# Optimization experiments

Hardware: AMD Instinct MI355X
Metric: run time of the kernel (lower is better)

The kernel has to match this reference:

```python
import jax, jax.numpy as jnp
import numpy as np

B, C, T, H, K = 512, 64, 512, 128, 16
EPS_BN = 1e-5


def setup_inputs() -> dict:
    key = jax.random.key(0)
    ks = jax.random.split(key, 8)
    s = 0.05
    return {
        "x": jax.random.normal(ks[0], (B, C, T), jnp.float32),
        "conv1_w": jax.random.normal(ks[1], (H, C, 3), jnp.float32) * s,
        "conv1_b": jnp.zeros((H,), jnp.float32),
        "conv2_w": jax.random.normal(ks[2], (H, H, 3), jnp.float32) * s,
        "conv2_b": jnp.zeros((H,), jnp.float32),
        "bnt1_g": jnp.ones((H,), jnp.float32), "bnt1_b": jnp.zeros((H,), jnp.float32),
        "bnt2_g": jnp.ones((H,), jnp.float32), "bnt2_b": jnp.zeros((H,), jnp.float32),
        "W1": jax.random.normal(ks[3], (T, H), jnp.float32) * s, "b1": jnp.zeros((H,), jnp.float32),
        "g1": jnp.ones((H,), jnp.float32), "be1": jnp.zeros((H,), jnp.float32),
        "W2": jax.random.normal(ks[4], (H, H), jnp.float32) * s, "b2": jnp.zeros((H,), jnp.float32),
        "g2": jnp.ones((H,), jnp.float32), "be2": jnp.zeros((H,), jnp.float32),
        "W3": jax.random.normal(ks[5], (H, H), jnp.float32) * s, "b3": jnp.zeros((H,), jnp.float32),
        "g3": jnp.ones((H,), jnp.float32), "be3": jnp.zeros((H,), jnp.float32),
    }


def _bn_nc(z, g, b):
    # BatchNorm1d on (N, C) with batch statistics (training-mode normalization)
    m = z.mean(0)
    v = z.var(0)
    return (z - m) * jax.lax.rsqrt(v + EPS_BN) * g + b


def _bn_ncl(z, g, b):
    # BatchNorm1d on (N, C, L)
    m = z.mean((0, 2), keepdims=True)
    v = z.var((0, 2), keepdims=True)
    return (z - m) * jax.lax.rsqrt(v + EPS_BN) * g[None, :, None] + b[None, :, None]


def _conv1d(z, w, b):
    y = jax.lax.conv_general_dilated(z, w, (1,), "SAME",
                                     dimension_numbers=("NCH", "OIH", "NCH"))
    return y + b[None, :, None]


def _forward(x, conv1_w, conv1_b, conv2_w, conv2_b, bnt1_g, bnt1_b, bnt2_g, bnt2_b,
             W1, b1, g1, be1, W2, b2, g2, be2, W3, b3, g3, be3):
    # temporal branch: computed but unused in the output (faithful to the source)
    ht = jax.nn.relu(_bn_ncl(_conv1d(x, conv1_w, conv1_b), bnt1_g, bnt1_b))
    ht = jax.nn.relu(_bn_ncl(_conv1d(ht, conv2_w, conv2_b), bnt2_g, bnt2_b))

    # dynamic graph: cosine similarity averaged over batch, top-k neighbors per channel
    xn = x / jnp.maximum(jnp.linalg.norm(x, axis=2, keepdims=True), 1e-12)
    sim = jnp.einsum("bct,bdt->cd", xn, xn) / x.shape[0]  # (C, C)
    _, nbr = jax.lax.top_k(sim, K)                        # (C, K)
    src = jnp.repeat(jnp.arange(C), K)                    # (C*K,)
    dst = nbr.reshape(-1)                                 # (C*K,)
    offs = (jnp.arange(B) * C)[:, None]
    N = B * C
    sl = jnp.arange(N)
    # edge_index[0]=source node i, edge_index[1]=its top-k neighbor; plus GCN self-loops
    es = jnp.concatenate([(src[None, :] + offs).reshape(-1), sl])
    ed = jnp.concatenate([(dst[None, :] + offs).reshape(-1), sl])

    deg = jax.ops.segment_sum(jnp.ones(es.shape[0], x.dtype), ed, num_segments=N)
    dinv = jax.lax.rsqrt(deg)  # deg >= 1 due to self-loops
    enorm = dinv[es] * dinv[ed]

    def gcn(h, W, b):
        hw = h @ W
        return jax.ops.segment_sum(hw[es] * enorm[:, None], ed, num_segments=N) + b

    # source does permute(0,2,1).view(B*C, T): a flat reshape of the (B, T, C) tensor
    nodes = jnp.transpose(x, (0, 2, 1)).reshape(N, T)
    h = jax.nn.relu(_bn_nc(gcn(nodes, W1, b1), g1, be1))
    h = jax.nn.relu(_bn_nc(gcn(h, W2, b2), g2, be2))
    h = jax.nn.relu(_bn_nc(gcn(h, W3, b3), g3, be3))
    return h.reshape(B, C * H)


def reference(x, conv1_w, conv1_b, conv2_w, conv2_b, bnt1_g, bnt1_b, bnt2_g, bnt2_b,
              W1, b1, g1, be1, W2, b2, g2, be2, W3, b3, g3, be3):
    return _forward(x, conv1_w, conv1_b, conv2_w, conv2_b, bnt1_g, bnt1_b,
                    bnt2_g, bnt2_b, W1, b1, g1, be1, W2, b2, g2, be2,
                    W3, b3, g3, be3)
```

## Files before the change

### kernel.cpp

```cpp
#include <hip/hip_runtime.h>
#include <math.h>

#define B_  512
#define C_  64
#define T_  512
#define H_  128
#define N_  (B_*C_)

typedef unsigned int   uint_;
typedef unsigned short ushort_;
typedef unsigned long long ull_;

typedef __attribute__((ext_vector_type(8))) short bf8v;
typedef __attribute__((ext_vector_type(4))) float f4v;

#define OFF_SIMP   0u
#define OFF_Z2     0u
#define OFF_Z1     8388608u
#define OFF_Z3     16777216u
#define OFF_WT1    25165824u
#define OFF_WT2    25296896u
#define OFF_WT3    25329664u
#define OFF_MASKS  25362432u
#define OFF_BNPART 25406464u
#define OFF_BNP2   25930752u
#define OFF_XH     33554432u

__device__ __forceinline__ ushort_ f2bf(float f) {
    uint_ u = __float_as_uint(f);
    u = (u + 0x7FFFu + ((u >> 16) & 1u)) >> 16;
    return (ushort_)u;
}
__device__ __forceinline__ float bf2f(ushort_ s) {
    return __uint_as_float(((uint_)s) << 16);
}

__device__ __forceinline__ void gload_lds16(const void* g, void* l) {
    __builtin_amdgcn_global_load_lds(
        (const __attribute__((address_space(1))) void*)g,
        (__attribute__((address_space(3))) void*)l, 16, 0, 0);
}

__device__ __forceinline__ void m_preamble_wave0(const ull_* __restrict__ masks,
                                                 ull_* nbrmS, float* dvS, int t)
{
    if (t < 64) {
        ull_ mask = masks[t];
        nbrmS[t] = mask;
        int deg = 1;
#pragma unroll
        for (int d = 0; d < 64; ++d) {
            ull_ bal = __ballot((int)((mask >> d) & 1ull));
            if (t == d) deg += (int)__popcll(bal);
        }
        dvS[t] = 1.0f / sqrtf((float)deg);
    }
}

__device__ __forceinline__ void m_build(const ull_* nbrmS, const float* dvS,
                                        int t, uint_ m8[8])
{
    const int d = t >> 2, q = t & 3;
    const float dvd = dvS[d];
#pragma unroll
    for (int p = 0; p < 8; ++p) {
        int c0 = 16 * q + 2 * p, c1 = c0 + 1;
        float w0 = (float)((int)((nbrmS[c0] >> d) & 1ull) + (c0 == d ? 1 : 0));
        float w1 = (float)((int)((nbrmS[c1] >> d) & 1ull) + (c1 == d ? 1 : 0));
        m8[p] = (uint_)f2bf(w0 * dvS[c0] * dvd) |
                ((uint_)f2bf(w1 * dvS[c1] * dvd) << 16);
    }
}

__global__ __launch_bounds__(256) void k_gramw(const float* __restrict__ x,
    float* __restrict__ simpart, ushort_* __restrict__ Xhg,
    const float* __restrict__ W1, const float* __restrict__ W2,
    const float* __restrict__ W3,
    ushort_* __restrict__ Wt1, ushort_* __restrict__ Wt2, ushort_* __restrict__ Wt3)
{
    __shared__ __align__(16) char smem[35584];
    __shared__ float  gd[64];
    __shared__ double rn[64];
    const int blk = blockIdx.x;
    const int t = threadIdx.x;

    if (blk < 512) {
        ushort_* Xh = (ushort_*)smem;
        ushort_* Xl = (ushort_*)(smem + 17408);
        const int b = blk;
        const int w = t >> 6, l = t & 63;
        const int lr = l & 15, lg = l >> 4;
        const int r0 = (w >> 1) * 2, c0 = (w & 1) * 2;

        f4v acc[2][2];
#pragma unroll
        for (int i = 0; i < 2; ++i)
#pragma unroll
            for (int j = 0; j < 2; ++j) acc[i][j] = (f4v)0.f;

        const float* xb = x + (size_t)b * (C_ * T_);

        for (int j = 0; j < 4; ++j) {
#pragma unroll
            for (int it = 0; it < 8; ++it) {
                int i = t + 256 * it;
                int c = i >> 5, t4 = i & 31;
                float4 v = *(const float4*)&xb[(size_t)c * T_ + 128 * j + 4 * t4];
                ushort_ h0 = f2bf(v.x), h1 = f2bf(v.y), h2 = f2bf(v.z), h3 = f2bf(v.w);
                uint2 ph;
                ph.x = (uint_)h0 | ((uint_)h1 << 16);
                ph.y = (uint_)h2 | ((uint_)h3 << 16);
                float e0 = v.x - bf2f(h0), e1 = v.y - bf2f(h1);
                float e2 = v.z - bf2f(h2), e3 = v.w - bf2f(h3);
                uint2 pl;
                pl.x = (uint_)f2bf(e0) | ((uint_)f2bf(e1) << 16);
                pl.y = (uint_)f2bf(e2) | ((uint_)f2bf(e3) << 16);
                *(uint2*)&Xh[c * 136 + 4 * t4] = ph;
                *(uint2*)&Xl[c * 136 + 4 * t4] = pl;
                *(uint2*)&Xhg[(((size_t)(b * 64 + c)) << 9) + 128 * j + 4 * t4] = ph;
            }
            __syncthreads();

#pragma unroll
            for (int s = 0; s < 4; ++s) {
                bf8v ah[2], al[2], bh[2], bl[2];
#pragma unroll
                for (int i = 0; i < 2; ++i) {
                    ah[i] = *(const bf8v*)&Xh[(16 * (r0 + i) + lr) * 136 + 32 * s + 8 * lg];
                    al[i] = *(const bf8v*)&Xl[(16 * (r0 + i) + lr) * 136 + 32 * s + 8 * lg];
                    bh[i] = *(const bf8v*)&Xh[(16 * (c0 + i) + lr) * 136 + 32 * s + 8 * lg];
                    bl[i] = *(const bf8v*)&Xl[(16 * (c0 + i) + lr) * 136 + 32 * s + 8 * lg];
                }
#pragma unroll
                for (int i = 0; i < 2; ++i)
#pragma unroll
                    for (int jj = 0; jj < 2; ++jj) {
                        acc[i][jj] = __builtin_amdgcn_mfma_f32_16x16x32_bf16(ah[i], bh[jj], acc[i][jj], 0, 0, 0);
                        acc[i][jj] = __builtin_amdgcn_mfma_f32_16x16x32_bf16(ah[i], bl[jj], acc[i][jj], 0, 0, 0);
                        acc[i][jj] = __builtin_amdgcn_mfma_f32_16x16x32_bf16(al[i], bh[jj], acc[i][jj], 0, 0, 0);
                    }
            }
            __syncthreads();
        }

        if (r0 == c0) {
#pragma unroll
            for (int d = 0; d < 2; ++d)
                if (lg == (lr >> 2)) gd[16 * (r0 + d) + lr] = acc[d][d][lr & 3];
        }
        __syncthreads();
        if (t < 64) rn[t] = 1.0 / fmax(sqrt((double)gd[t]), 1e-12);
        __syncthreads();

        float* sp = simpart + (size_t)b * 4096;
#pragma unroll
        for (int i = 0; i < 2; ++i)
#pragma unroll
            for (int jj = 0; jj < 2; ++jj)
#pragma unroll
                for (int reg = 0; reg < 4; ++reg) {
                    int rc = 16 * (r0 + i) + 4 * lg + reg;
                    int cc = 16 * (c0 + jj) + lr;
                    sp[rc * 64 + cc] = (float)((double)acc[i][jj][reg] * rn[rc] * rn[cc]);
                }
    } else {
        float* L = (float*)smem;
        const int pblk = blk - 512;
        if (pblk < 8) {
            for (int it = 0; it < 8; ++it) {
                int i = t + 256 * it;
                int ri = i >> 5, f4 = i & 31;
                int m = ri >> 3, cr = ri & 7;
                *(float4*)&L[ri * 132 + 4 * f4] =
                    *(const float4*)&W1[(size_t)(64 * m + 8 * pblk + cr) * H_ + 4 * f4];
            }
            __syncthreads();
            int f = t >> 1, half = t & 1;
            uint_ buf[16];
#pragma unroll
            for (int jj = 0; jj < 16; ++jj) {
                int k0 = 32 * half + 2 * jj;
                int c0 = k0 >> 3, m0 = k0 & 7;
                int c1 = (k0 + 1) >> 3, m1 = (k0 + 1) & 7;
                buf[jj] = (uint_)f2bf(L[(m0 * 8 + c0) * 132 + f]) |
                          ((uint_)f2bf(L[(m1 * 8 + c1) * 132 + f]) << 16);
            }
            ushort_* dst = Wt1 + (size_t)f * 512 + 64 * pblk + 32 * half;
#pragma unroll
            for (int q = 0; q < 4; ++q) {
                uint4 vv = {buf[4 * q], buf[4 * q + 1], buf[4 * q + 2], buf[4 * q + 3]};
                *(uint4*)&dst[8 * q] = vv;
            }
        } else {
            const float* W = (pblk < 10) ? W2 : W3;
            ushort_*     O = (pblk < 10) ? Wt2 : Wt3;
            int kb = (pblk - 8) & 1;
            for (int it = 0; it < 8; ++it) {
                int i = t + 256 * it;
                int ri = i >> 5, f4 = i & 31;
                *(float4*)&L[ri * 132 + 4 * f4] =
                    *(const float4*)&W[(size_t)(64 * kb + ri) * H_ + 4 * f4];
            }
            __syncthreads();
            int f = t >> 1, half = t & 1;
            uint_ buf[16];
#pragma unroll
            for (int jj = 0; jj < 16; ++jj) {
                int k0 = 32 * half + 2 * jj;
                buf[jj] = (uint_)f2bf(L[k0 * 132 + f]) |
                          ((uint_)f2bf(L[(k0 + 1) * 132 + f]) << 16);
            }
            ushort_* dst = O + (size_t)f * 128 + 64 * kb + 32 * half;
#pragma unroll
            for (int q = 0; q < 4; ++q) {
                uint4 vv = {buf[4 * q], buf[4 * q + 1], buf[4 * q + 2], buf[4 * q + 3]};
                *(uint4*)&dst[8 * q] = vv;
            }
        }
    }
}

__global__ __launch_bounds__(1024) void k_simrank(const float* __restrict__ simpart,
                                                  ull_* __restrict__ masks)
{
    __shared__ double part[16][64];
    __shared__ double sd[64];
    const int c = blockIdx.x;
    const int t = threadIdx.x;
    const int d = t & 63, g = t >> 6;

    double a = 0.0;
    const float* sp = simpart + (size_t)c * 64 + d;
    for (int i = 0; i < 32; ++i)
        a += (double)sp[(size_t)(g + 16 * i) * 4096];
    part[g][d] = a;
    __syncthreads();

    if (t < 64) {
        double s = 0.0;
#pragma unroll
        for (int q = 0; q < 16; ++q) s += part[q][t];
        sd[t] = s;
        int rank = 0;
#pragma unroll
        for (int dp = 0; dp < 64; ++dp) {
            double w = sd[dp];
            rank += (w > s || (w == s && dp < t)) ? 1 : 0;
        }
        ull_ m = __ballot(rank < 16);
        if (t == 0) masks[c] = m;
    }
}

__device__ __forceinline__ void mfma_epilogue(char* smem, int b, int t,
    f4v acc[8], const float* __restrict__ bias, const uint_ m8[8],
    ushort_* __restrict__ Zout, float* __restrict__ bnpart)
{
    const int l = t & 63, w = t >> 6;
    const int lr = l & 15, lg = l >> 4;

    ushort_* Yt  = (ushort_*)smem;
    ushort_* Ml  = (ushort_*)(smem + 22528);
    ushort_* Zst = (ushort_*)(smem + 33792);

#pragma unroll
    for (int nt = 0; nt < 8; ++nt) {
        uint2 p;
        p.x = (uint_)f2bf(acc[nt][0]) | ((uint_)f2bf(acc[nt][1]) << 16);
        p.y = (uint_)f2bf(acc[nt][2]) | ((uint_)f2bf(acc[nt][3]) << 16);
        *(uint2*)&Yt[(16 * nt + lr) * 88 + 16 * w + 4 * lg] = p;
    }
    {
        const int d = t >> 2, q = t & 3;
        uint4 v0 = {m8[0], m8[1], m8[2], m8[3]};
        uint4 v1 = {m8[4], m8[5], m8[6], m8[7]};
        *(uint4*)&Ml[d * 88 + 16 * q]     = v0;
        *(uint4*)&Ml[d * 88 + 16 * q + 8] = v1;
    }
    __syncthreads();

    f4v z[8];
#pragma unroll
    for (int nt = 0; nt < 8; ++nt) z[nt] = (f4v)0.f;
#pragma unroll
    for (int cs = 0; cs < 2; ++cs) {
        bf8v mf = *(const bf8v*)&Ml[(16 * w + lr) * 88 + 32 * cs + 8 * lg];
#pragma unroll
        for (int nt = 0; nt < 8; ++nt) {
            bf8v yf = *(const bf8v*)&Yt[(16 * nt + lr) * 88 + 32 * cs + 8 * lg];
            z[nt] = __builtin_amdgcn_mfma_f32_16x16x32_bf16(mf, yf, z[nt], 0, 0, 0);
        }
    }

#pragma unroll
    for (int nt = 0; nt < 8; ++nt) {
        float bv = bias[16 * nt + lr];
#pragma unroll
        for (int reg = 0; reg < 4; ++reg)
            Zst[(16 * w + 4 * lg + reg) * 136 + 16 * nt + lr] = f2bf(z[nt][reg] + bv);
    }
    __syncthreads();

    if (t < 128) {
        float s = 0.f, s2 = 0.f;
        for (int r = 0; r < 64; ++r) {
            float v = bf2f(Zst[r * 136 + t]);
            s += v; s2 += v * v;
        }
        bnpart[b * 256 + t]       = s;
        bnpart[b * 256 + 128 + t] = s2;
    }
#pragma unroll
    for (int it = 0; it < 4; ++it) {
        int i = t + 256 * it;
        int r = i >> 4, seg = i & 15;
        *(uint4*)&Zout[((size_t)(b * 64 + r)) * 128 + 8 * seg] =
            *(const uint4*)&Zst[r * 136 + 8 * seg];
    }
}

__global__ __launch_bounds__(256) void k_mgemm1(const ushort_* __restrict__ Xh,
    const ushort_* __restrict__ Wt, const float* __restrict__ bias,
    const ull_* __restrict__ masks, ushort_* __restrict__ Zout,
    float* __restrict__ bnpart)
{
    __shared__ __align__(16) char smem[51456];
    __shared__ ull_  nbrmS[64];
    __shared__ float dvS[64];
    ushort_* Al = (ushort_*)smem;
    ushort_* Wl = (ushort_*)(smem + 16384);

    const int b = blockIdx.x;
    const int t = threadIdx.x;
    const int l = t & 63, w = t >> 6;
    const int lr = l & 15, lg = l >> 4;

    m_preamble_wave0(masks, nbrmS, dvS, t);

    f4v acc[8];
#pragma unroll
    for (int nt = 0; nt < 8; ++nt) acc[nt] = (f4v)0.f;

    for (int j = 0; j < 4; ++j) {
        {
            const char* asrc = (const char*)(Xh + (((size_t)(b * 64 + 16 * j)) << 9)) + t * 16;
            char* adst = smem + t * 16;
#pragma unroll
            for (int i2 = 0; i2 < 4; ++i2)
                gload_lds16(asrc + i2 * 4096, adst + i2 * 4096);
        }
        {
            const int fr = t >> 4, seg = t & 15;
            const char* wsrc = (const char*)(Wt + (size_t)fr * 512 + 128 * j + seg * 8);
            char* wdst = smem + 16384 + t * 16;
#pragma unroll
            for (int i2 = 0; i2 < 8; ++i2)
                gload_lds16(wsrc + i2 * 16384, wdst + i2 * 4096);
        }
        __syncthreads();
#pragma unroll
        for (int s = 0; s < 4; ++s) {
            bf8v af = *(const bf8v*)&Al[(4 * s + lg) * 512 + 128 * w + 8 * lr];
#pragma unroll
            for (int nt = 0; nt < 8; ++nt) {
                bf8v bfv = *(const bf8v*)&Wl[(16 * nt + lr) * 128 + 32 * s + 8 * lg];
                acc[nt] = __builtin_amdgcn_mfma_f32_16x16x32_bf16(af, bfv, acc[nt], 0, 0, 0);
            }
        }
        __syncthreads();
    }

    uint_ m8[8];
    m_build(nbrmS, dvS, t, m8);
    mfma_epilogue(smem, b, t, acc, bias, m8, Zout, bnpart);
}

__global__ __launch_bounds__(256) void k_mgemm23(const ushort_* __restrict__ Zin,
    const double* __restrict__ bnp2, const float* __restrict__ g,
    const float* __restrict__ be, const ushort_* __restrict__ Wt,
    const float* __restrict__ bias, const ull_* __restrict__ masks,
    ushort_* __restrict__ Zout, float* __restrict__ bnpart)
{
    __shared__ __align__(16) char smem[52224];
    __shared__ float ssL[256];
    __shared__ ull_  nbrmS[64];
    __shared__ float dvS[64];
    ushort_* Al = (ushort_*)smem;
    ushort_* Wl = (ushort_*)(smem + 17408);

    const int b = blockIdx.x;
    const int t = threadIdx.x;
    const int l = t & 63, w = t >> 6;
    const int lr = l & 15, lg = l >> 4;

    {
        double* sumsL = (double*)smem;
        double a = 0.0;
        for (int q = 0; q < 32; ++q) a += bnp2[(size_t)q * 256 + t];
        sumsL[t] = a;
        m_preamble_wave0(masks, nbrmS, dvS, t);
        __syncthreads();
        if (t < 128) {
            double s = sumsL[t], s2 = sumsL[128 + t];
            double mean = s * (1.0 / 32768.0);
            double var  = s2 * (1.0 / 32768.0) - mean * mean;
            double rstd = 1.0 / sqrt(var + 1e-5);
            float sc = (float)((double)g[t] * rstd);
            ssL[t]       = sc;
            ssL[128 + t] = (float)((double)be[t] - mean * (double)sc);
        }
        __syncthreads();
    }

    {
        const char* wsrc = (const char*)Wt + t * 16;
        char* wdst = smem + 17408 + t * 16;
#pragma unroll
        for (int i2 = 0; i2 < 8; ++i2)
            gload_lds16(wsrc + i2 * 4096, wdst + i2 * 4096);
    }

    f4v acc[8];
#pragma unroll
    for (int nt = 0; nt < 8; ++nt) acc[nt] = (f4v)0.f;

#pragma unroll
    for (int it = 0; it < 4; ++it) {
        int i = t + 256 * it;
        int r = i >> 4, seg = i & 15;
        uint4 v = *(const uint4*)&Zin[((size_t)(b * 64 + r)) * 128 + 8 * seg];
        uint_ w0[4] = {v.x, v.y, v.z, v.w};
        uint_ o[4];
#pragma unroll
        for (int p = 0; p < 4; ++p) {
            int f0 = 8 * seg + 2 * p;
            float z0 = bf2f((ushort_)(w0[p] & 0xFFFF));
            float z1 = bf2f((ushort_)(w0[p] >> 16));
            float h0 = fmaxf(fmaf(z0, ssL[f0],     ssL[128 + f0]),     0.f);
            float h1 = fmaxf(fmaf(z1, ssL[f0 + 1], ssL[128 + f0 + 1]), 0.f);
            o[p] = (uint_)f2bf(h0) | ((uint_)f2bf(h1) << 16);
        }
        uint4 ov = {o[0], o[1], o[2], o[3]};
        *(uint4*)&Al[r * 136 + 8 * seg] = ov;
    }
    __syncthreads();
#pragma unroll
    for (int s = 0; s < 4; ++s) {
        bf8v af = *(const bf8v*)&Al[(16 * w + lr) * 136 + 32 * s + 8 * lg];
#pragma unroll
        for (int nt = 0; nt < 8; ++nt) {
            bf8v bfv = *(const bf8v*)&Wl[(16 * nt + lr) * 128 + 32 * s + 8 * lg];
            acc[nt] = __builtin_amdgcn_mfma_f32_16x16x32_bf16(af, bfv, acc[nt], 0, 0, 0);
        }
    }
    __syncthreads();

    uint_ m8[8];
    m_build(nbrmS, dvS, t, m8);
    mfma_epilogue(smem, b, t, acc, bias, m8, Zout, bnpart);
}

__global__ __launch_bounds__(256) void k_bnA(const float* __restrict__ bnpart,
                                             double* __restrict__ bnp2)
{
    const int t = threadIdx.x, g = blockIdx.x;
    double a = 0.0;
    for (int i = 0; i < 16; ++i)
        a += (double)bnpart[(size_t)(16 * g + i) * 256 + t];
    bnp2[(size_t)g * 256 + t] = a;
}

__global__ __launch_bounds__(256) void k_out(const ushort_* __restrict__ Z,
    const double* __restrict__ bnp2, const float* __restrict__ g,
    const float* __restrict__ be, float* __restrict__ out)
{
    __shared__ double sumsL[256];
    __shared__ float  ssL[256];
    const int b = blockIdx.x;
    const int t = threadIdx.x;

    double a = 0.0;
    for (int q = 0; q < 32; ++q) a += bnp2[(size_t)q * 256 + t];
    sumsL[t] = a;
    __syncthreads();
    if (t < 128) {
        double s = sumsL[t], s2 = sumsL[128 + t];
        double mean = s * (1.0 / 32768.0);
        double var  = s2 * (1.0 / 32768.0) - mean * mean;
        double rstd = 1.0 / sqrt(var + 1e-5);
        float sc = (float)((double)g[t] * rstd);
        ssL[t]       = sc;
        ssL[128 + t] = (float)((double)be[t] - mean * (double)sc);
    }
    __syncthreads();

    const size_t base = (size_t)b * 64 * 128;
#pragma unroll
    for (int it = 0; it < 8; ++it) {
        int i = t + 256 * it;
        int r = i >> 5, s = i & 31;
        uint2 v = *(const uint2*)&Z[base + (size_t)r * 128 + 4 * s];
        float4 sc = *(const float4*)&ssL[4 * s];
        float4 sh = *(const float4*)&ssL[128 + 4 * s];
        float z0 = bf2f((ushort_)(v.x & 0xFFFF));
        float z1 = bf2f((ushort_)(v.x >> 16));
        float z2 = bf2f((ushort_)(v.y & 0xFFFF));
        float z3 = bf2f((ushort_)(v.y >> 16));
        float4 o;
        o.x = fmaxf(fmaf(z0, sc.x, sh.x), 0.f);
        o.y = fmaxf(fmaf(z1, sc.y, sh.y), 0.f);
        o.z = fmaxf(fmaf(z2, sc.z, sh.z), 0.f);
        o.w = fmaxf(fmaf(z3, sc.w, sh.w), 0.f);
        *(float4*)&out[base + (size_t)r * 128 + 4 * s] = o;
    }
}

extern "C" void kernel_launch(void* const* d_in, const int* in_sizes, int n_in,
                              void* d_out, int out_size, void* d_ws, size_t ws_size,
                              hipStream_t stream)
{
    (void)in_sizes; (void)n_in; (void)out_size; (void)ws_size;

    const float* x   = (const float*)d_in[0];
    const float* W1  = (const float*)d_in[9];
    const float* b1  = (const float*)d_in[10];
    const float* g1  = (const float*)d_in[11];
    const float* be1 = (const float*)d_in[12];
    const float* W2  = (const float*)d_in[13];
    const float* b2  = (const float*)d_in[14];
    const float* g2  = (const float*)d_in[15];
    const float* be2 = (const float*)d_in[16];
    const float* W3  = (const float*)d_in[17];
    const float* b3  = (const float*)d_in[18];
    const float* g3  = (const float*)d_in[19];
    const float* be3 = (const float*)d_in[20];

    char* ws = (char*)d_ws;
    float*   simp   = (float*)(ws + OFF_SIMP);
    ull_*    masks  = (ull_*)(ws + OFF_MASKS);
    ushort_* Wt1    = (ushort_*)(ws + OFF_WT1);
    ushort_* Wt2    = (ushort_*)(ws + OFF_WT2);
    ushort_* Wt3    = (ushort_*)(ws + OFF_WT3);
    float*   bnpart = (float*)(ws + OFF_BNPART);
    double*  bnp2   = (double*)(ws + OFF_BNP2);
    ushort_* Xh     = (ushort_*)(ws + OFF_XH);
    ushort_* Z1     = (ushort_*)(ws + OFF_Z1);
    ushort_* Z2     = (ushort_*)(ws + OFF_Z2);
    ushort_* Z3     = (ushort_*)(ws + OFF_Z3);
    float*   out    = (float*)d_out;

    k_gramw<<<dim3(524), dim3(256), 0, stream>>>(x, simp, Xh, W1, W2, W3, Wt1, Wt2, Wt3);
    k_simrank<<<dim3(64), dim3(1024), 0, stream>>>(simp, masks);

    k_mgemm1<<<dim3(512), dim3(256), 0, stream>>>(Xh, Wt1, b1, masks, Z1, bnpart);
    k_bnA<<<dim3(32), dim3(256), 0, stream>>>(bnpart, bnp2);

    k_mgemm23<<<dim3(512), dim3(256), 0, stream>>>(Z1, bnp2, g1, be1, Wt2, b2, masks, Z2, bnpart);
    k_bnA<<<dim3(32), dim3(256), 0, stream>>>(bnpart, bnp2);

    k_mgemm23<<<dim3(512), dim3(256), 0, stream>>>(Z2, bnp2, g2, be2, Wt3, b3, masks, Z3, bnpart);
    k_bnA<<<dim3(32), dim3(256), 0, stream>>>(bnpart, bnp2);

    k_out<<<dim3(512), dim3(256), 0, stream>>>(Z3, bnp2, g3, be3, out);
}
```

Measured before the change: 99.02 us.

## Fuse first GCN weight GEMM into Gram kernel and use atomic fixed-point BN sums

The Gram-matrix kernel now also multiplies the bf16 x tile by W1 while the tile sits in LDS. It writes a small per-batch Y1 = X·W1 product instead of the full bf16 copy of x, so the first graph-mixing step reads Y1 and needs only a 64x64 mixing GEMM. The separate BN partial-reduction kernels are removed: per-block sums are added with 64-bit integer atomics in a fixed-point scale, and a memset zeroes the accumulators. This cuts launches and memory traffic, at the cost of atomic contention, fixed-point precision limits, and a changed rounding order (W1 is applied before neighbour mixing).

```diff
diff --git a/kernel.cpp b/kernel.cpp
--- a/kernel.cpp
+++ b/kernel.cpp
@@ -13,6 +13,8 @@
 
 typedef __attribute__((ext_vector_type(8))) short bf8v;
 typedef __attribute__((ext_vector_type(4))) float f4v;
+
+#define BN_SCALE 4194304.0
 
 #define OFF_SIMP   0u
 #define OFF_Z2     0u
@@ -22,9 +24,8 @@
 #define OFF_WT2    25296896u
 #define OFF_WT3    25329664u
 #define OFF_MASKS  25362432u
-#define OFF_BNPART 25406464u
-#define OFF_BNP2   25930752u
-#define OFF_XH     33554432u
+#define OFF_BNACC  25406464u
+#define OFF_Y1T    33554432u
 
 __device__ __forceinline__ ushort_ f2bf(float f) {
     uint_ u = __float_as_uint(f);
@@ -72,151 +73,163 @@
     }
 }
 
-__global__ __launch_bounds__(256) void k_gramw(const float* __restrict__ x,
-    float* __restrict__ simpart, ushort_* __restrict__ Xhg,
-    const float* __restrict__ W1, const float* __restrict__ W2,
-    const float* __restrict__ W3,
+__global__ __launch_bounds__(256) void k_prepw(const float* __restrict__ W1,
+    const float* __restrict__ W2, const float* __restrict__ W3,
     ushort_* __restrict__ Wt1, ushort_* __restrict__ Wt2, ushort_* __restrict__ Wt3)
 {
-    __shared__ __align__(16) char smem[35584];
+    __shared__ float L[64 * 132];
+    const int blk = blockIdx.x, t = threadIdx.x;
+
+    if (blk < 8) {
+        for (int it = 0; it < 8; ++it) {
+            int i = t + 256 * it;
+            int ri = i >> 5, f4 = i & 31;
+            int m = ri >> 3, cr = ri & 7;
+            *(float4*)&L[ri * 132 + 4 * f4] =
+                *(const float4*)&W1[(size_t)(64 * m + 8 * blk + cr) * H_ + 4 * f4];
+        }
+        __syncthreads();
+        int f = t >> 1, half = t & 1;
+        uint_ buf[16];
+#pragma unroll
+        for (int jj = 0; jj < 16; ++jj) {
+            int k0 = 32 * half + 2 * jj;
+            int c0 = k0 >> 3, m0 = k0 & 7;
+            int c1 = (k0 + 1) >> 3, m1 = (k0 + 1) & 7;
+            buf[jj] = (uint_)f2bf(L[(m0 * 8 + c0) * 132 + f]) |
+                      ((uint_)f2bf(L[(m1 * 8 + c1) * 132 + f]) << 16);
+        }
+        ushort_* dst = Wt1 + (size_t)f * 512 + 64 * blk + 32 * half;
+#pragma unroll
+        for (int q = 0; q < 4; ++q) {
+            uint4 vv = {buf[4 * q], buf[4 * q + 1], buf[4 * q + 2], buf[4 * q + 3]};
+            *(uint4*)&dst[8 * q] = vv;
+        }
+    } else {
+        const float* W = (blk < 10) ? W2 : W3;
+        ushort_*     O = (blk < 10) ? Wt2 : Wt3;
+        int kb = (blk - 8) & 1;
+        for (int it = 0; it < 8; ++it) {
+            int i = t + 256 * it;
+            int ri = i >> 5, f4 = i & 31;
+            *(float4*)&L[ri * 132 + 4 * f4] =
+                *(const float4*)&W[(size_t)(64 * kb + ri) * H_ + 4 * f4];
+        }
+        __syncthreads();
+        int f = t >> 1, half = t & 1;
+        uint_ buf[16];
+#pragma unroll
+        for (int jj = 0; jj < 16; ++jj) {
+            int k0 = 32 * half + 2 * jj;
+            buf[jj] = (uint_)f2bf(L[k0 * 132 + f]) |
+                      ((uint_)f2bf(L[(k0 + 1) * 132 + f]) << 16);
+        }
+        ushort_* dst = O + (size_t)f * 128 + 64 * kb + 32 * half;
+#pragma unroll
+        for (int q = 0; q < 4; ++q) {
+            uint4 vv = {buf[4 * q], buf[4 * q + 1], buf[4 * q + 2], buf[4 * q + 3]};
+            *(uint4*)&dst[8 * q] = vv;
+        }
+    }
+}
+
+__global__ __launch_bounds__(512, 4) void k_gramg1(const float* __restrict__ x,
+    float* __restrict__ simpart, const ushort_* __restrict__ Wt,
+    ushort_* __restrict__ Y1t)
+{
+    __shared__ ushort_ Xh[64 * 136];
+    __shared__ ushort_ Xl[64 * 136];
+    __shared__ ushort_ Y1f[128 * 72];
     __shared__ float  gd[64];
     __shared__ double rn[64];
-    const int blk = blockIdx.x;
+
+    const int b = blockIdx.x;
     const int t = threadIdx.x;
-
-    if (blk < 512) {
-        ushort_* Xh = (ushort_*)smem;
-        ushort_* Xl = (ushort_*)(smem + 17408);
-        const int b = blk;
-        const int w = t >> 6, l = t & 63;
-        const int lr = l & 15, lg = l >> 4;
-        const int r0 = (w >> 1) * 2, c0 = (w & 1) * 2;
-
-        f4v acc[2][2];
-#pragma unroll
-        for (int i = 0; i < 2; ++i)
-#pragma unroll
-            for (int j = 0; j < 2; ++j) acc[i][j] = (f4v)0.f;
-
-        const float* xb = x + (size_t)b * (C_ * T_);
-
-        for (int j = 0; j < 4; ++j) {
-#pragma unroll
-            for (int it = 0; it < 8; ++it) {
-                int i = t + 256 * it;
-                int c = i >> 5, t4 = i & 31;
-                float4 v = *(const float4*)&xb[(size_t)c * T_ + 128 * j + 4 * t4];
-                ushort_ h0 = f2bf(v.x), h1 = f2bf(v.y), h2 = f2bf(v.z), h3 = f2bf(v.w);
-                uint2 ph;
-                ph.x = (uint_)h0 | ((uint_)h1 << 16);
-                ph.y = (uint_)h2 | ((uint_)h3 << 16);
-                float e0 = v.x - bf2f(h0), e1 = v.y - bf2f(h1);
-                float e2 = v.z - bf2f(h2), e3 = v.w - bf2f(h3);
-                uint2 pl;
-                pl.x = (uint_)f2bf(e0) | ((uint_)f2bf(e1) << 16);
-                pl.y = (uint_)f2bf(e2) | ((uint_)f2bf(e3) << 16);
-                *(uint2*)&Xh[c * 136 + 4 * t4] = ph;
-                *(uint2*)&Xl[c * 136 + 4 * t4] = pl;
-                *(uint2*)&Xhg[(((size_t)(b * 64 + c)) << 9) + 128 * j + 4 * t4] = ph;
+    const int w = t >> 6, l = t & 63;
+    const int lr = l & 15, lg = l >> 4;
+    const int rp = w >> 1, ch = w & 1;
+
+    f4v gacc[2];
+#pragma unroll
+    for (int i = 0; i < 2; ++i) gacc[i] = (f4v)0.f;
+
+    const float* xb = x + (size_t)b * (C_ * T_);
+
+    for (int j = 0; j < 4; ++j) {
+#pragma unroll
+        for (int it = 0; it < 4; ++it) {
+            int i = t + 512 * it;
+            int c = i >> 5, t4 = i & 31;
+            float4 v = *(const float4*)&xb[(size_t)c * T_ + 128 * j + 4 * t4];
+            ushort_ h0 = f2bf(v.x), h1 = f2bf(v.y), h2 = f2bf(v.z), h3 = f2bf(v.w);
+            uint2 ph;
+            ph.x = (uint_)h0 | ((uint_)h1 << 16);
+            ph.y = (uint_)h2 | ((uint_)h3 << 16);
+            float e0 = v.x - bf2f(h0), e1 = v.y - bf2f(h1);
+            float e2 = v.z - bf2f(h2), e3 = v.w - bf2f(h3);
+            uint2 pl;
+            pl.x = (uint_)f2bf(e0) | ((uint_)f2bf(e1) << 16);
+            pl.y = (uint_)f2bf(e2) | ((uint_)f2bf(e3) << 16);
+            *(uint2*)&Xh[c * 136 + 4 * t4] = ph;
+            *(uint2*)&Xl[c * 136 + 4 * t4] = pl;
+        }
+        __syncthreads();
+
+#pragma unroll
+        for (int s = 0; s < 4; ++s) {
+            bf8v ah = *(const bf8v*)&Xh[(16 * rp + lr) * 136 + 32 * s + 8 * lg];
+            bf8v al = *(const bf8v*)&Xl[(16 * rp + lr) * 136 + 32 * s + 8 * lg];
+#pragma unroll
+            for (int i = 0; i < 2; ++i) {
+                const int ct = 2 * ch + i;
+                bf8v bh = *(const bf8v*)&Xh[(16 * ct + lr) * 136 + 32 * s + 8 * lg];
+                bf8v bl = *(const bf8v*)&Xl[(16 * ct + lr) * 136 + 32 * s + 8 * lg];
+                gacc[i] = __builtin_amdgcn_mfma_f32_16x16x32_bf16(ah, bh, gacc[i], 0, 0, 0);
+                gacc[i] = __builtin_amdgcn_mfma_f32_16x16x32_bf16(ah, bl, gacc[i], 0, 0, 0);
+                gacc[i] = __builtin_amdgcn_mfma_f32_16x16x32_bf16(al, bh, gacc[i], 0, 0, 0);
             }
-            __syncthreads();
-
-#pragma unroll
-            for (int s = 0; s < 4; ++s) {
-                bf8v ah[2], al[2], bh[2], bl[2];
-#pragma unroll
-                for (int i = 0; i < 2; ++i) {
-                    ah[i] = *(const bf8v*)&Xh[(16 * (r0 + i) + lr) * 136 + 32 * s + 8 * lg];
-                    al[i] = *(const bf8v*)&Xl[(16 * (r0 + i) + lr) * 136 + 32 * s + 8 * lg];
-                    bh[i] = *(const bf8v*)&Xh[(16 * (c0 + i) + lr) * 136 + 32 * s + 8 * lg];
-                    bl[i] = *(const bf8v*)&Xl[(16 * (c0 + i) + lr) * 136 + 32 * s + 8 * lg];
-                }
-#pragma unroll
-                for (int i = 0; i < 2; ++i)
-#pragma unroll
-                    for (int jj = 0; jj < 2; ++jj) {
-                        acc[i][jj] = __builtin_amdgcn_mfma_f32_16x16x32_bf16(ah[i], bh[jj], acc[i][jj], 0, 0, 0);
-                        acc[i][jj] = __builtin_amdgcn_mfma_f32_16x16x32_bf16(ah[i], bl[jj], acc[i][jj], 0, 0, 0);
-                        acc[i][jj] = __builtin_amdgcn_mfma_f32_16x16x32_bf16(al[i], bh[jj], acc[i][jj], 0, 0, 0);
-                    }
+        }
+
+        {
+            f4v ga = (f4v)0.f;
+#pragma unroll 4
+            for (int s = 0; s < 16; ++s) {
+                bf8v af = *(const bf8v*)&Xh[(4 * s + lg) * 136 + 8 * lr];
+                bf8v bfv = *(const bf8v*)&Wt[(size_t)(16 * w + lr) * 512 + 32 * s + 8 * lg];
+                ga = __builtin_amdgcn_mfma_f32_16x16x32_bf16(af, bfv, ga, 0, 0, 0);
             }
-            __syncthreads();
-        }
-
-        if (r0 == c0) {
-#pragma unroll
-            for (int d = 0; d < 2; ++d)
-                if (lg == (lr >> 2)) gd[16 * (r0 + d) + lr] = acc[d][d][lr & 3];
+#pragma unroll
+            for (int reg = 0; reg < 4; ++reg)
+                Y1f[(16 * w + lr) * 72 + 16 * j + 4 * lg + reg] = f2bf(ga[reg]);
         }
         __syncthreads();
-        if (t < 64) rn[t] = 1.0 / fmax(sqrt((double)gd[t]), 1e-12);
-        __syncthreads();
-
-        float* sp = simpart + (size_t)b * 4096;
-#pragma unroll
-        for (int i = 0; i < 2; ++i)
-#pragma unroll
-            for (int jj = 0; jj < 2; ++jj)
-#pragma unroll
-                for (int reg = 0; reg < 4; ++reg) {
-                    int rc = 16 * (r0 + i) + 4 * lg + reg;
-                    int cc = 16 * (c0 + jj) + lr;
-                    sp[rc * 64 + cc] = (float)((double)acc[i][jj][reg] * rn[rc] * rn[cc]);
-                }
-    } else {
-        float* L = (float*)smem;
-        const int pblk = blk - 512;
-        if (pblk < 8) {
-            for (int it = 0; it < 8; ++it) {
-                int i = t + 256 * it;
-                int ri = i >> 5, f4 = i & 31;
-                int m = ri >> 3, cr = ri & 7;
-                *(float4*)&L[ri * 132 + 4 * f4] =
-                    *(const float4*)&W1[(size_t)(64 * m + 8 * pblk + cr) * H_ + 4 * f4];
-            }
-            __syncthreads();
-            int f = t >> 1, half = t & 1;
-            uint_ buf[16];
-#pragma unroll
-            for (int jj = 0; jj < 16; ++jj) {
-                int k0 = 32 * half + 2 * jj;
-                int c0 = k0 >> 3, m0 = k0 & 7;
-                int c1 = (k0 + 1) >> 3, m1 = (k0 + 1) & 7;
-                buf[jj] = (uint_)f2bf(L[(m0 * 8 + c0) * 132 + f]) |
-                          ((uint_)f2bf(L[(m1 * 8 + c1) * 132 + f]) << 16);
-            }
-            ushort_* dst = Wt1 + (size_t)f * 512 + 64 * pblk + 32 * half;
-#pragma unroll
-            for (int q = 0; q < 4; ++q) {
-                uint4 vv = {buf[4 * q], buf[4 * q + 1], buf[4 * q + 2], buf[4 * q + 3]};
-                *(uint4*)&dst[8 * q] = vv;
-            }
-        } else {
-            const float* W = (pblk < 10) ? W2 : W3;
-            ushort_*     O = (pblk < 10) ? Wt2 : Wt3;
-            int kb = (pblk - 8) & 1;
-            for (int it = 0; it < 8; ++it) {
-                int i = t + 256 * it;
-                int ri = i >> 5, f4 = i & 31;
-                *(float4*)&L[ri * 132 + 4 * f4] =
-                    *(const float4*)&W[(size_t)(64 * kb + ri) * H_ + 4 * f4];
-            }
-            __syncthreads();
-            int f = t >> 1, half = t & 1;
-            uint_ buf[16];
-#pragma unroll
-            for (int jj = 0; jj < 16; ++jj) {
-                int k0 = 32 * half + 2 * jj;
-                buf[jj] = (uint_)f2bf(L[k0 * 132 + f]) |
-                          ((uint_)f2bf(L[(k0 + 1) * 132 + f]) << 16);
-            }
-            ushort_* dst = O + (size_t)f * 128 + 64 * kb + 32 * half;
-#pragma unroll
-            for (int q = 0; q < 4; ++q) {
-                uint4 vv = {buf[4 * q], buf[4 * q + 1], buf[4 * q + 2], buf[4 * q + 3]};
-                *(uint4*)&dst[8 * q] = vv;
-            }
-        }
+    }
+
+    {
+        const int di = rp - 2 * ch;
+        if ((di == 0 || di == 1) && lg == (lr >> 2))
+            gd[16 * rp + lr] = gacc[di][lr & 3];
+    }
+    __syncthreads();
+    if (t < 64) rn[t] = 1.0 / fmax(sqrt((double)gd[t]), 1e-12);
+    __syncthreads();
+
+    float* sp = simpart + (size_t)b * 4096;
+#pragma unroll
+    for (int i = 0; i < 2; ++i)
+#pragma unroll
+        for (int reg = 0; reg < 4; ++reg) {
+            int rc = 16 * rp + 4 * lg + reg;
+            int cc = 16 * (2 * ch + i) + lr;
+            sp[rc * 64 + cc] = (float)((double)gacc[i][reg] * rn[rc] * rn[cc]);
+        }
+
+#pragma unroll
+    for (int it = 0; it < 2; ++it) {
+        int i = t + 512 * it;
+        int f = i >> 3, seg = i & 7;
+        *(uint4*)&Y1t[(size_t)b * 8192 + f * 64 + 8 * seg] =
+            *(const uint4*)&Y1f[f * 72 + 8 * seg];
     }
 }
 
@@ -254,7 +267,7 @@
 
 __device__ __forceinline__ void mfma_epilogue(char* smem, int b, int t,
     f4v acc[8], const float* __restrict__ bias, const uint_ m8[8],
-    ushort_* __restrict__ Zout, float* __restrict__ bnpart)
+    ushort_* __restrict__ Zout, ull_* __restrict__ bnacc)
 {
     const int l = t & 63, w = t >> 6;
     const int lr = l & 15, lg = l >> 4;
@@ -307,8 +320,8 @@
             float v = bf2f(Zst[r * 136 + t]);
             s += v; s2 += v * v;
         }
-        bnpart[b * 256 + t]       = s;
-        bnpart[b * 256 + 128 + t] = s2;
+        atomicAdd(&bnacc[t],       (ull_)(long long)__double2ll_rn((double)s  * BN_SCALE));
+        atomicAdd(&bnacc[128 + t], (ull_)(long long)__double2ll_rn((double)s2 * BN_SCALE));
     }
 #pragma unroll
     for (int it = 0; it < 4; ++it) {
@@ -319,16 +332,16 @@
     }
 }
 
-__global__ __launch_bounds__(256) void k_mgemm1(const ushort_* __restrict__ Xh,
-    const ushort_* __restrict__ Wt, const float* __restrict__ bias,
-    const ull_* __restrict__ masks, ushort_* __restrict__ Zout,
-    float* __restrict__ bnpart)
-{
-    __shared__ __align__(16) char smem[51456];
+__global__ __launch_bounds__(256) void k_mix1(const ushort_* __restrict__ Y1t,
+    const float* __restrict__ bias, const ull_* __restrict__ masks,
+    ushort_* __restrict__ Zout, ull_* __restrict__ bnacc)
+{
+    __shared__ __align__(16) char smem[51200];
     __shared__ ull_  nbrmS[64];
     __shared__ float dvS[64];
-    ushort_* Al = (ushort_*)smem;
-    ushort_* Wl = (ushort_*)(smem + 16384);
+    ushort_* Yt  = (ushort_*)smem;
+    ushort_* Ml  = (ushort_*)(smem + 22528);
+    ushort_* Zst = (ushort_*)(smem + 33792);
 
     const int b = blockIdx.x;
     const int t = threadIdx.x;
@@ -337,51 +350,73 @@
 
     m_preamble_wave0(masks, nbrmS, dvS, t);
 
-    f4v acc[8];
-#pragma unroll
-    for (int nt = 0; nt < 8; ++nt) acc[nt] = (f4v)0.f;
-
-    for (int j = 0; j < 4; ++j) {
-        {
-            const char* asrc = (const char*)(Xh + (((size_t)(b * 64 + 16 * j)) << 9)) + t * 16;
-            char* adst = smem + t * 16;
-#pragma unroll
-            for (int i2 = 0; i2 < 4; ++i2)
-                gload_lds16(asrc + i2 * 4096, adst + i2 * 4096);
-        }
-        {
-            const int fr = t >> 4, seg = t & 15;
-            const char* wsrc = (const char*)(Wt + (size_t)fr * 512 + 128 * j + seg * 8);
-            char* wdst = smem + 16384 + t * 16;
-#pragma unroll
-            for (int i2 = 0; i2 < 8; ++i2)
-                gload_lds16(wsrc + i2 * 16384, wdst + i2 * 4096);
-        }
-        __syncthreads();
-#pragma unroll
-        for (int s = 0; s < 4; ++s) {
-            bf8v af = *(const bf8v*)&Al[(4 * s + lg) * 512 + 128 * w + 8 * lr];
-#pragma unroll
-            for (int nt = 0; nt < 8; ++nt) {
-                bf8v bfv = *(const bf8v*)&Wl[(16 * nt + lr) * 128 + 32 * s + 8 * lg];
-                acc[nt] = __builtin_amdgcn_mfma_f32_16x16x32_bf16(af, bfv, acc[nt], 0, 0, 0);
-            }
-        }
-        __syncthreads();
-    }
+#pragma unroll
+    for (int it = 0; it < 8; ++it) {
+        int i = t + 256 * it;
+        int f = i >> 3, seg = i & 7;
+        *(uint4*)&Yt[f * 88 + 8 * seg] =
+            *(const uint4*)&Y1t[(size_t)b * 8192 + f * 64 + 8 * seg];
+    }
+    __syncthreads();
 
     uint_ m8[8];
     m_build(nbrmS, dvS, t, m8);
-    mfma_epilogue(smem, b, t, acc, bias, m8, Zout, bnpart);
+    {
+        const int d = t >> 2, q = t & 3;
+        uint4 v0 = {m8[0], m8[1], m8[2], m8[3]};
+        uint4 v1 = {m8[4], m8[5], m8[6], m8[7]};
+        *(uint4*)&Ml[d * 88 + 16 * q]     = v0;
+        *(uint4*)&Ml[d * 88 + 16 * q + 8] = v1;
+    }
+    __syncthreads();
+
+    f4v z[8];
+#pragma unroll
+    for (int nt = 0; nt < 8; ++nt) z[nt] = (f4v)0.f;
+#pragma unroll
+    for (int cs = 0; cs < 2; ++cs) {
+        bf8v mf = *(const bf8v*)&Ml[(16 * w + lr) * 88 + 32 * cs + 8 * lg];
+#pragma unroll
+        for (int nt = 0; nt < 8; ++nt) {
+            bf8v yf = *(const bf8v*)&Yt[(16 * nt + lr) * 88 + 32 * cs + 8 * lg];
+            z[nt] = __builtin_amdgcn_mfma_f32_16x16x32_bf16(mf, yf, z[nt], 0, 0, 0);
+        }
+    }
+
+#pragma unroll
+    for (int nt = 0; nt < 8; ++nt) {
+        float bv = bias[16 * nt + lr];
+#pragma unroll
+        for (int reg = 0; reg < 4; ++reg)
+            Zst[(16 * w + 4 * lg + reg) * 136 + 16 * nt + lr] = f2bf(z[nt][reg] + bv);
+    }
+    __syncthreads();
+
+    if (t < 128) {
+        float s = 0.f, s2 = 0.f;
+        for (int r = 0; r < 64; ++r) {
+            float v = bf2f(Zst[r * 136 + t]);
+            s += v; s2 += v * v;
+        }
+        atomicAdd(&bnacc[t],       (ull_)(long long)__double2ll_rn((double)s  * BN_SCALE));
+        atomicAdd(&bnacc[128 + t], (ull_)(long long)__double2ll_rn((double)s2 * BN_SCALE));
+    }
+#pragma unroll
+    for (int it = 0; it < 4; ++it) {
+        int i = t + 256 * it;
+        int r = i >> 4, seg = i & 15;
+        *(uint4*)&Zout[((size_t)(b * 64 + r)) * 128 + 8 * seg] =
+            *(const uint4*)&Zst[r * 136 + 8 * seg];
+    }
 }
 
 __global__ __launch_bounds__(256) void k_mgemm23(const ushort_* __restrict__ Zin,
-    const double* __restrict__ bnp2, const float* __restrict__ g,
+    const ull_* __restrict__ bnaccIn, const float* __restrict__ g,
     const float* __restrict__ be, const ushort_* __restrict__ Wt,
     const float* __restrict__ bias, const ull_* __restrict__ masks,
-    ushort_* __restrict__ Zout, float* __restrict__ bnpart)
-{
-    __shared__ __align__(16) char smem[52224];
+    ushort_* __restrict__ Zout, ull_* __restrict__ bnaccOut)
+{
+    __shared__ __align__(16) char smem[51200];
     __shared__ float ssL[256];
     __shared__ ull_  nbrmS[64];
     __shared__ float dvS[64];
@@ -394,10 +429,10 @@
     const int lr = l & 15, lg = l >> 4;
 
     {
+        long long ll = (long long)bnaccIn[t];
+        double sv = (double)ll * (1.0 / BN_SCALE);
         double* sumsL = (double*)smem;
-        double a = 0.0;
-        for (int q = 0; q < 32; ++q) a += bnp2[(size_t)q * 256 + t];
-        sumsL[t] = a;
+        sumsL[t] = sv;
         m_preamble_wave0(masks, nbrmS, dvS, t);
         __syncthreads();
         if (t < 128) {
@@ -457,21 +492,11 @@
 
     uint_ m8[8];
     m_build(nbrmS, dvS, t, m8);
-    mfma_epilogue(smem, b, t, acc, bias, m8, Zout, bnpart);
-}
-
-__global__ __launch_bounds__(256) void k_bnA(const float* __restrict__ bnpart,
-                                             double* __restrict__ bnp2)
-{
-    const int t = threadIdx.x, g = blockIdx.x;
-    double a = 0.0;
-    for (int i = 0; i < 16; ++i)
-        a += (double)bnpart[(size_t)(16 * g + i) * 256 + t];
-    bnp2[(size_t)g * 256 + t] = a;
+    mfma_epilogue(smem, b, t, acc, bias, m8, Zout, bnaccOut);
 }
 
 __global__ __launch_bounds__(256) void k_out(const ushort_* __restrict__ Z,
-    const double* __restrict__ bnp2, const float* __restrict__ g,
+    const ull_* __restrict__ bnaccIn, const float* __restrict__ g,
     const float* __restrict__ be, float* __restrict__ out)
 {
     __shared__ double sumsL[256];
@@ -479,9 +504,7 @@
     const int b = blockIdx.x;
     const int t = threadIdx.x;
 
-    double a = 0.0;
-    for (int q = 0; q < 32; ++q) a += bnp2[(size_t)q * 256 + t];
-    sumsL[t] = a;
+    sumsL[t] = (double)(long long)bnaccIn[t] * (1.0 / BN_SCALE);
     __syncthreads();
     if (t < 128) {
         double s = sumsL[t], s2 = sumsL[128 + t];
@@ -541,25 +564,23 @@
     ushort_* Wt1    = (ushort_*)(ws + OFF_WT1);
     ushort_* Wt2    = (ushort_*)(ws + OFF_WT2);
     ushort_* Wt3    = (ushort_*)(ws + OFF_WT3);
-    float*   bnpart = (float*)(ws + OFF_BNPART);
-    double*  bnp2   = (double*)(ws + OFF_BNP2);
-    ushort_* Xh     = (ushort_*)(ws + OFF_XH);
+    ull_*    bnacc1 = (ull_*)(ws + OFF_BNACC);
+    ull_*    bnacc2 = bnacc1 + 256;
+    ull_*    bnacc3 = bnacc1 + 512;
+    ushort_* Y1t    = (ushort_*)(ws + OFF_Y1T);
     ushort_* Z1     = (ushort_*)(ws + OFF_Z1);
     ushort_* Z2     = (ushort_*)(ws + OFF_Z2);
     ushort_* Z3     = (ushort_*)(ws + OFF_Z3);
     float*   out    = (float*)d_out;
 
-    k_gramw<<<dim3(524), dim3(256), 0, stream>>>(x, simp, Xh, W1, W2, W3, Wt1, Wt2, Wt3);
+    hipMemsetAsync(ws + OFF_BNACC, 0, 3 * 256 * sizeof(ull_), stream);
+
+    k_prepw<<<dim3(12), dim3(256), 0, stream>>>(W1, W2, W3, Wt1, Wt2, Wt3);
+    k_gramg1<<<dim3(512), dim3(512), 0, stream>>>(x, simp, Wt1, Y1t);
     k_simrank<<<dim3(64), dim3(1024), 0, stream>>>(simp, masks);
 
-    k_mgemm1<<<dim3(512), dim3(256), 0, stream>>>(Xh, Wt1, b1, masks, Z1, bnpart);
-    k_bnA<<<dim3(32), dim3(256), 0, stream>>>(bnpart, bnp2);
-
-    k_mgemm23<<<dim3(512), dim3(256), 0, stream>>>(Z1, bnp2, g1, be1, Wt2, b2, masks, Z2, bnpart);
-    k_bnA<<<dim3(32), dim3(256), 0, stream>>>(bnpart, bnp2);
-
-    k_mgemm23<<<dim3(512), dim3(256), 0, stream>>>(Z2, bnp2, g2, be2, Wt3, b3, masks, Z3, bnpart);
-    k_bnA<<<dim3(32), dim3(256), 0, stream>>>(bnpart, bnp2);
-
-    k_out<<<dim3(512), dim3(256), 0, stream>>>(Z3, bnp2, g3, be3, out);
-}
+    k_mix1<<<dim3(512), dim3(256), 0, stream>>>(Y1t, b1, masks, Z1, bnacc1);
+    k_mgemm23<<<dim3(512), dim3(256), 0, stream>>>(Z1, bnacc1, g1, be1, Wt2, b2, masks, Z2, bnacc2);
+    k_mgemm23<<<dim3(512), dim3(256), 0, stream>>>(Z2, bnacc2, g2, be2, Wt3, b3, masks, Z3, bnacc3);
+    k_out<<<dim3(512), dim3(256), 0, stream>>>(Z3, bnacc3, g3, be3, out);
+}
```

After: 129.6 us. 1.31x slower.
